# Performance work log

Measured on AMD Instinct MI355X. Metric: run time of the kernel, lower is better.

The kernel has to match this reference:

```python
import jax, jax.numpy as jnp
import numpy as np

N_NODES = 100000
N_EDGES = 3200000
IN_DIM, HID_DIM, OUT_DIM = 128, 64, 2


def setup_inputs() -> dict:
    key = jax.random.key(0)
    k1, k2, k3, k4 = jax.random.split(key, 4)
    x = jax.random.normal(k1, (N_NODES, IN_DIM), dtype=jnp.float32)
    edge_index = jax.random.randint(k2, (2, N_EDGES), 0, N_NODES, dtype=jnp.int64)
    # GCNConv weights (glorot-style scale) and zero biases
    W1 = jax.random.normal(k3, (IN_DIM, HID_DIM), dtype=jnp.float32) / np.sqrt(IN_DIM)
    b1 = jnp.zeros((HID_DIM,), dtype=jnp.float32)
    W2 = jax.random.normal(k4, (HID_DIM, OUT_DIM), dtype=jnp.float32) / np.sqrt(HID_DIM)
    b2 = jnp.zeros((OUT_DIM,), dtype=jnp.float32)
    return {"x": x, "edge_index": edge_index, "W1": W1, "b1": b1, "W2": W2, "b2": b2}


def _gcn_norm(edge_index, num_nodes):
    # PyG GCNConv default: add self-loops, symmetric normalization deg^-1/2.
    loops = jnp.arange(num_nodes, dtype=edge_index.dtype)
    src = jnp.concatenate([edge_index[0], loops])  # [E+N]
    dst = jnp.concatenate([edge_index[1], loops])  # [E+N]
    deg = jax.ops.segment_sum(jnp.ones_like(dst, dtype=jnp.float32), dst,
                              num_segments=num_nodes)  # in-degree incl. self-loop
    dinv = jnp.where(deg > 0, jax.lax.rsqrt(deg), 0.0)
    norm = dinv[src] * dinv[dst]  # [E+N]
    return src, dst, norm


def _gcn_conv(h, W, b, src, dst, norm, num_nodes):
    h = h @ W                              # dense transform first (smaller dim)
    msg = h[src] * norm[:, None]           # gather + scale: [E+N, d]
    out = jax.ops.segment_sum(msg, dst, num_segments=num_nodes)  # scatter-add
    return out + b


def reference(x, edge_index, W1, b1, W2, b2):
    n = x.shape[0]
    src, dst, norm = _gcn_norm(edge_index, n)
    h = _gcn_conv(x, W1, b1, src, dst, norm, n)
    h = jax.nn.relu(h)
    return _gcn_conv(h, W2, b2, src, dst, norm, n)
```

## Files before the change

kernel.cpp:

```cpp
#include <hip/hip_runtime.h>
#include <hip/hip_bf16.h>


#define N_NODES 100000
#define IN_DIM 128
#define HID_DIM 64
#define OUT_DIM 2
#define NB 391
#define BCAP 12288
#define CROUNDS 12
#define CHUNK 8192
#define ZROW N_NODES

typedef short bf16x8 __attribute__((ext_vector_type(8)));
typedef float f32x4 __attribute__((ext_vector_type(4)));

__device__ __forceinline__ unsigned short f2bf(float x) {
    unsigned int u = __float_as_uint(x);
    unsigned int r = (u + 0x7FFFu + ((u >> 16) & 1u)) >> 16;
    return (unsigned short)r;
}
__device__ __forceinline__ float bflo(unsigned int u) { return __uint_as_float(u << 16); }
__device__ __forceinline__ float bfhi(unsigned int u) { return __uint_as_float(u & 0xFFFF0000u); }
__device__ __forceinline__ f32x4 vlo(uint4 r) {
    return (f32x4){bflo(r.x), bflo(r.y), bflo(r.z), bflo(r.w)};
}
__device__ __forceinline__ f32x4 vhi(uint4 r) {
    return (f32x4){bfhi(r.x), bfhi(r.y), bfhi(r.z), bfhi(r.w)};
}
__device__ __forceinline__ int wave_incl_scan(int v, int laneid) {
#pragma unroll
    for (int off = 1; off < 64; off <<= 1) {
        int u = __shfl_up(v, off);
        if (laneid >= off) v += u;
    }
    return v;
}

__global__ __launch_bounds__(512) void part_kernel(const int* __restrict__ ei,
                                                   int* __restrict__ gCursor,
                                                   int* __restrict__ part, int E) {
    __shared__ int hist[512], lrow[512], gbase[512], lcur[512];
    __shared__ int lpk[CHUNK];
    __shared__ short lbkt[CHUNK];
    __shared__ int wsum[8], wofs[8];
    const int t = threadIdx.x;
    const int lane = t & 63, wv = t >> 6;
    const int base = blockIdx.x * CHUNK;
    const int cntC = min(CHUNK, E - base);

    hist[t] = 0;
    __syncthreads();

    int s[16], d[16];
    bool val[16];
    if (base + CHUNK <= E) {
#pragma unroll
        for (int i = 0; i < 4; ++i) {
            int4 sv = ((const int4*)(ei + base))[t + i * 512];
            int4 dv = ((const int4*)(ei + E + base))[t + i * 512];
            s[i * 4 + 0] = sv.x; s[i * 4 + 1] = sv.y; s[i * 4 + 2] = sv.z; s[i * 4 + 3] = sv.w;
            d[i * 4 + 0] = dv.x; d[i * 4 + 1] = dv.y; d[i * 4 + 2] = dv.z; d[i * 4 + 3] = dv.w;
            val[i * 4 + 0] = val[i * 4 + 1] = val[i * 4 + 2] = val[i * 4 + 3] = true;
        }
    } else {
#pragma unroll
        for (int i = 0; i < 16; ++i) {
            int e = base + t + i * 512;
            val[i] = (e < E);
            if (val[i]) {
                s[i] = ei[e];
                d[i] = ei[E + e];
            }
        }
    }
#pragma unroll
    for (int i = 0; i < 16; ++i)
        if (val[i]) atomicAdd(&hist[d[i] >> 8], 1);
    __syncthreads();

    int v = hist[t];
    int inc = wave_incl_scan(v, lane);
    if (lane == 63) wsum[wv] = inc;
    __syncthreads();
    if (t < 64) {
        int w = (t < 8) ? wsum[t] : 0;
        int wi = wave_incl_scan(w, t);
        if (t < 8) wofs[t] = wi - w;
    }
    __syncthreads();
    int excl = inc - v + wofs[wv];
    if (t < NB && v > 0) {
        int old = atomicAdd(&gCursor[t], v);
        gbase[t] = t * BCAP + old;
    }
    lcur[t] = excl;
    lrow[t] = excl;
    __syncthreads();

#pragma unroll
    for (int i = 0; i < 16; ++i) {
        if (val[i]) {
            int b = d[i] >> 8;
            int pos = atomicAdd(&lcur[b], 1);
            lpk[pos] = s[i] | ((d[i] & 255) << 20);
            lbkt[pos] = (short)b;
        }
    }
    __syncthreads();

    for (int i = t; i < cntC; i += 512) {
        int b = lbkt[i];
        int g = gbase[b] + (i - lrow[b]);
        if (g < (b + 1) * BCAP)
            part[g] = lpk[i];
    }
}

__global__ __launch_bounds__(1024) void csr_kernel(const int* __restrict__ part,
                                                   const int* __restrict__ gCursor,
                                                   int* __restrict__ cnt,
                                                   float* __restrict__ dinv,
                                                   int* __restrict__ rowptr,
                                                   int* __restrict__ csr_src, int n) {
    __shared__ int wcnt[16][256];
    __shared__ int wsum[4], wofs[4];
    const int b = blockIdx.x, t = threadIdx.x;
    const int lane = t & 63, wv = t >> 6;
    const int start = b * BCAP;
    const int count = min(gCursor[b], BCAP);

    for (int i = t; i < 16 * 256; i += 1024) ((int*)wcnt)[i] = 0;
    __syncthreads();

    int pk[CROUNDS];
    bool val[CROUNDS];
#pragma unroll
    for (int k = 0; k < CROUNDS; ++k) {
        int i = t + k * 1024;
        val[k] = (i < count);
        pk[k] = val[k] ? part[start + i] : 0;
        if (val[k]) atomicAdd(&wcnt[wv][(pk[k] >> 20) & 255], 1);
    }
    __syncthreads();

    int v = 0, pv = 0;
    if (t < 256) {
        int sum = 0;
#pragma unroll
        for (int w = 0; w < 16; ++w) sum += wcnt[w][t];
        v = sum;
        pv = (v + 7) & ~7;
    }
    int inc = 0;
    if (t < 256) {
        inc = wave_incl_scan(pv, lane);
        if (lane == 63) wsum[wv] = inc;
    }
    __syncthreads();
    if (t < 64) {
        int w = (t < 4) ? wsum[t] : 0;
        int wi = wave_incl_scan(w, t);
        if (t < 4) wofs[t] = wi - w;
    }
    __syncthreads();
    if (t < 256) {
        int excl = inc - pv + wofs[wv];
        int node = (b << 8) + t;
        if (node < n) {
            cnt[node] = v;
            dinv[node] = rsqrtf((float)v + 1.0f);
            rowptr[node] = start + excl;
        }
        for (int j = v; j < pv; ++j) csr_src[start + excl + j] = ZROW;
        int run = excl;
#pragma unroll
        for (int w = 0; w < 16; ++w) {
            int c = wcnt[w][t];
            wcnt[w][t] = run;
            run += c;
        }
    }
    __syncthreads();

#pragma unroll
    for (int k = 0; k < CROUNDS; ++k) {
        if (val[k]) {
            int pos = atomicAdd(&wcnt[wv][(pk[k] >> 20) & 255], 1);
            csr_src[start + pos] = pk[k] & 0xFFFFF;
        }
    }
}

__global__ __launch_bounds__(256) void gemm1_kernel(const float* __restrict__ x,
                                                    const float* __restrict__ W1,
                                                    const float* __restrict__ dinv,
                                                    unsigned short* __restrict__ hsb, int n) {
    __shared__ unsigned short sX[64 * 136];
    __shared__ unsigned short sW[64 * 136];
    const int tid = threadIdx.x;
    const int rbase = blockIdx.x * 64;

    if (blockIdx.x == 0 && tid < 8)
        ((float4*)&hsb[(unsigned)ZROW * HID_DIM])[tid] = make_float4(0.f, 0.f, 0.f, 0.f);

    for (int i = tid; i < 2048; i += 256) {
        int k = i >> 4, cq = (i & 15) << 2;
        float4 v = ((const float4*)W1)[i];
        sW[(cq + 0) * 136 + k] = f2bf(v.x);
        sW[(cq + 1) * 136 + k] = f2bf(v.y);
        sW[(cq + 2) * 136 + k] = f2bf(v.z);
        sW[(cq + 3) * 136 + k] = f2bf(v.w);
    }
    for (int i = tid; i < 2048; i += 256) {
        int r = i >> 5, kq = (i & 31) << 2;
        int gr = rbase + r;
        float4 v = make_float4(0.f, 0.f, 0.f, 0.f);
        if (gr < n) v = ((const float4*)x)[gr * 32 + (i & 31)];
        ushort4 u;
        u.x = f2bf(v.x); u.y = f2bf(v.y); u.z = f2bf(v.z); u.w = f2bf(v.w);
        *(ushort4*)&sX[r * 136 + kq] = u;
    }
    __syncthreads();

    const int wave = tid >> 6, lane = tid & 63;
    const int quad = lane >> 4, l16 = lane & 15;
    const int rowoff = wave * 16;

    f32x4 acc[4];
#pragma unroll
    for (int t = 0; t < 4; ++t) acc[t] = (f32x4){0.f, 0.f, 0.f, 0.f};

#pragma unroll
    for (int k0 = 0; k0 < 128; k0 += 32) {
        bf16x8 a = *(const bf16x8*)&sX[(rowoff + l16) * 136 + k0 + quad * 8];
#pragma unroll
        for (int t = 0; t < 4; ++t) {
            bf16x8 b = *(const bf16x8*)&sW[(t * 16 + l16) * 136 + k0 + quad * 8];
            acc[t] = __builtin_amdgcn_mfma_f32_16x16x32_bf16(a, b, acc[t], 0, 0, 0);
        }
    }

#pragma unroll
    for (int r = 0; r < 4; ++r) {
        int grow = rbase + rowoff + quad * 4 + r;
        if (grow < n) {
            float di = dinv[grow];
#pragma unroll
            for (int t = 0; t < 4; ++t)
                hsb[grow * HID_DIM + t * 16 + l16] = f2bf(acc[t][r] * di);
        }
    }
}

__global__ __launch_bounds__(256) void agg1_kernel(const int* __restrict__ rowptr,
                                                   const int* __restrict__ cnt,
                                                   const int* __restrict__ csr_src,
                                                   const unsigned short* __restrict__ hsb,
                                                   const float* __restrict__ dinv,
                                                   const float* __restrict__ b1,
                                                   const float* __restrict__ W2,
                                                   float* __restrict__ hs2, int n) {
    const int node = blockIdx.x * 32 + (threadIdx.x >> 3);
    const int l = threadIdx.x & 7;
    const unsigned lofs = (unsigned)l * 8;
    const int start = rowptr[node];
    const int deg = cnt[node];
    const int iters = (deg + 7) >> 3;

    f32x4 alo = (f32x4){0.f, 0.f, 0.f, 0.f};
    f32x4 ahi = (f32x4){0.f, 0.f, 0.f, 0.f};

    const int4* qp = (const int4*)(csr_src + start);
    int4 ia = make_int4(ZROW, ZROW, ZROW, ZROW), ib = ia;
    if (iters > 0) { ia = qp[0]; ib = qp[1]; }
    for (int it = 0; it < iters; ++it) {
        const bool more = (it + 1 < iters);
        int4 na = more ? qp[2 * it + 2] : make_int4(ZROW, ZROW, ZROW, ZROW);
        int4 nb = more ? qp[2 * it + 3] : make_int4(ZROW, ZROW, ZROW, ZROW);
        uint4 r0 = *(const uint4*)&hsb[(unsigned)ia.x * HID_DIM + lofs];
        uint4 r1 = *(const uint4*)&hsb[(unsigned)ia.y * HID_DIM + lofs];
        uint4 r2 = *(const uint4*)&hsb[(unsigned)ia.z * HID_DIM + lofs];
        uint4 r3 = *(const uint4*)&hsb[(unsigned)ia.w * HID_DIM + lofs];
        uint4 r4 = *(const uint4*)&hsb[(unsigned)ib.x * HID_DIM + lofs];
        uint4 r5 = *(const uint4*)&hsb[(unsigned)ib.y * HID_DIM + lofs];
        uint4 r6 = *(const uint4*)&hsb[(unsigned)ib.z * HID_DIM + lofs];
        uint4 r7 = *(const uint4*)&hsb[(unsigned)ib.w * HID_DIM + lofs];
        alo += vlo(r0);  ahi += vhi(r0);
        alo += vlo(r1);  ahi += vhi(r1);
        alo += vlo(r2);  ahi += vhi(r2);
        alo += vlo(r3);  ahi += vhi(r3);
        alo += vlo(r4);  ahi += vhi(r4);
        alo += vlo(r5);  ahi += vhi(r5);
        alo += vlo(r6);  ahi += vhi(r6);
        alo += vlo(r7);  ahi += vhi(r7);
        ia = na; ib = nb;
    }

    float a[8];
    a[0] = alo[0]; a[1] = ahi[0]; a[2] = alo[1]; a[3] = ahi[1];
    a[4] = alo[2]; a[5] = ahi[2]; a[6] = alo[3]; a[7] = ahi[3];

    {
        uint4 raw = *(const uint4*)&hsb[(unsigned)node * HID_DIM + lofs];
        a[0] += bflo(raw.x); a[1] += bfhi(raw.x);
        a[2] += bflo(raw.y); a[3] += bfhi(raw.y);
        a[4] += bflo(raw.z); a[5] += bfhi(raw.z);
        a[6] += bflo(raw.w); a[7] += bfhi(raw.w);
    }

    float di = dinv[node];
    float4 bb0 = *(const float4*)&b1[l * 8];
    float4 bb1 = *(const float4*)&b1[l * 8 + 4];
    float t0 = fmaxf(fmaf(di, a[0], bb0.x), 0.0f);
    float t1 = fmaxf(fmaf(di, a[1], bb0.y), 0.0f);
    float t2 = fmaxf(fmaf(di, a[2], bb0.z), 0.0f);
    float t3 = fmaxf(fmaf(di, a[3], bb0.w), 0.0f);
    float t4 = fmaxf(fmaf(di, a[4], bb1.x), 0.0f);
    float t5 = fmaxf(fmaf(di, a[5], bb1.y), 0.0f);
    float t6 = fmaxf(fmaf(di, a[6], bb1.z), 0.0f);
    float t7 = fmaxf(fmaf(di, a[7], bb1.w), 0.0f);

    float4 w0 = *(const float4*)&W2[l * 16];
    float4 w1 = *(const float4*)&W2[l * 16 + 4];
    float4 w2 = *(const float4*)&W2[l * 16 + 8];
    float4 w3 = *(const float4*)&W2[l * 16 + 12];
    float p0 = t0 * w0.x + t1 * w0.z + t2 * w1.x + t3 * w1.z
             + t4 * w2.x + t5 * w2.z + t6 * w3.x + t7 * w3.z;
    float p1 = t0 * w0.y + t1 * w0.w + t2 * w1.y + t3 * w1.w
             + t4 * w2.y + t5 * w2.w + t6 * w3.y + t7 * w3.w;
    p0 += __shfl_xor(p0, 1);  p1 += __shfl_xor(p1, 1);
    p0 += __shfl_xor(p0, 2);  p1 += __shfl_xor(p1, 2);
    p0 += __shfl_xor(p0, 4);  p1 += __shfl_xor(p1, 4);

    if (l == 0) {
        *(float2*)&hs2[node * OUT_DIM] = make_float2(di * p0, di * p1);
    }
}

__global__ __launch_bounds__(256) void agg2_kernel(const int* __restrict__ rowptr,
                                                   const int* __restrict__ cnt,
                                                   const int* __restrict__ csr_src,
                                                   const float* __restrict__ hs2,
                                                   const float* __restrict__ dinv,
                                                   const float* __restrict__ b2,
                                                   float* __restrict__ out, int n) {
    int node = blockIdx.x * 16 + (threadIdx.x >> 4);
    int lane = threadIdx.x & 15;
    int start = rowptr[node];
    int deg = cnt[node];

    float a0 = 0.0f, a1 = 0.0f;
    for (int j = lane; j < deg; j += 16) {
        int s = csr_src[start + j];
        float2 v = *(const float2*)&hs2[s * OUT_DIM];
        a0 += v.x;
        a1 += v.y;
    }
#pragma unroll
    for (int off = 8; off > 0; off >>= 1) {
        a0 += __shfl_xor(a0, off);
        a1 += __shfl_xor(a1, off);
    }
    if (lane == 0) {
        float di = dinv[node];
        float2 self = *(const float2*)&hs2[node * OUT_DIM];
        out[node * OUT_DIM + 0] = di * (a0 + self.x) + b2[0];
        out[node * OUT_DIM + 1] = di * (a1 + self.y) + b2[1];
    }
}

extern "C" void kernel_launch(void* const* d_in, const int* in_sizes, int n_in,
                              void* d_out, int out_size, void* d_ws, size_t ws_size,
                              hipStream_t stream) {
    const float* x  = (const float*)d_in[0];
    const int*   ei = (const int*)d_in[1];
    const float* W1 = (const float*)d_in[2];
    const float* b1 = (const float*)d_in[3];
    const float* W2 = (const float*)d_in[4];
    const float* b2 = (const float*)d_in[5];
    float* out = (float*)d_out;

    const int n = N_NODES;
    const int E = in_sizes[1] / 2;

    char* ws = (char*)d_ws;
    int*   gCursor = (int*)  (ws + 0);
    int*   cnt     = (int*)  (ws + (1u << 20));
    float* dinv    = (float*)(ws + (2u << 20));
    int*   rowptr  = (int*)  (ws + (3u << 20));
    float* hs2     = (float*)(ws + (4u << 20));
    int*   part    = (int*)  (ws + (5u << 20));
    unsigned short* hsb = (unsigned short*)(ws + (5u << 20));
    int*   csr_src = (int*)  (ws + (25u << 20));

    hipMemsetAsync(gCursor, 0, NB * sizeof(int), stream);

    part_kernel<<<(E + CHUNK - 1) / CHUNK, 512, 0, stream>>>(ei, gCursor, part, E);
    csr_kernel<<<NB, 1024, 0, stream>>>(part, gCursor, cnt, dinv, rowptr, csr_src, n);

    gemm1_kernel<<<(n + 63) / 64, 256, 0, stream>>>(x, W1, dinv, hsb, n);
    agg1_kernel<<<n / 32, 256, 0, stream>>>(rowptr, cnt, csr_src, hsb, dinv, b1, W2, hs2, n);
    agg2_kernel<<<n / 16, 256, 0, stream>>>(rowptr, cnt, csr_src, hs2, dinv, b2, out, n);
}
```

Baseline: 232.2 us.

## Sort nodes by degree within block and widen agg1 gather to 16 edges

Inside agg1, each block now bitonic-sorts its 32 nodes by degree so that nodes with similar degree share a wavefront, which cuts divergence from uneven trip counts. The gather loop also handles 16 neighbour rows per iteration instead of 8, with CSR row padding raised to multiples of 16 to match. This puts more loads in flight per iteration. The cost is extra padding entries that point at the zero row, more register pressure, and a small sort plus block barrier per block.

```diff
diff --git a/kernel.cpp b/kernel.cpp
--- a/kernel.cpp
+++ b/kernel.cpp
@@ -150,7 +150,7 @@
 #pragma unroll
         for (int w = 0; w < 16; ++w) sum += wcnt[w][t];
         v = sum;
-        pv = (v + 7) & ~7;
+        pv = (v + 15) & ~15;
     }
     int inc = 0;
     if (t < 256) {
@@ -261,23 +261,49 @@
                                                    const float* __restrict__ b1,
                                                    const float* __restrict__ W2,
                                                    float* __restrict__ hs2, int n) {
-    const int node = blockIdx.x * 32 + (threadIdx.x >> 3);
-    const int l = threadIdx.x & 7;
+    __shared__ int sid[32];
+    const int tid = threadIdx.x;
+    const int nbase = blockIdx.x * 32;
+
+    if (tid < 32) {
+        int nd = nbase + tid;
+        int key = min(cnt[nd], 1023);
+        int v = (key << 17) | nd;
+#pragma unroll
+        for (int k = 2; k <= 32; k <<= 1) {
+#pragma unroll
+            for (int j = k >> 1; j > 0; j >>= 1) {
+                int u = __shfl_xor(v, j);
+                bool asc = ((tid & k) == 0);
+                bool low = ((tid & j) == 0);
+                int mn = min(v, u), mx = max(v, u);
+                v = (asc == low) ? mn : mx;
+            }
+        }
+        sid[tid] = v & 0x1FFFF;
+    }
+    __syncthreads();
+
+    const int node = sid[tid >> 3];
+    const int l = tid & 7;
     const unsigned lofs = (unsigned)l * 8;
     const int start = rowptr[node];
     const int deg = cnt[node];
-    const int iters = (deg + 7) >> 3;
+    const int iters = (deg + 15) >> 4;
 
     f32x4 alo = (f32x4){0.f, 0.f, 0.f, 0.f};
     f32x4 ahi = (f32x4){0.f, 0.f, 0.f, 0.f};
 
+    const int4 Z4 = make_int4(ZROW, ZROW, ZROW, ZROW);
     const int4* qp = (const int4*)(csr_src + start);
-    int4 ia = make_int4(ZROW, ZROW, ZROW, ZROW), ib = ia;
-    if (iters > 0) { ia = qp[0]; ib = qp[1]; }
+    int4 ia = Z4, ib = Z4, ic = Z4, id = Z4;
+    if (iters > 0) { ia = qp[0]; ib = qp[1]; ic = qp[2]; id = qp[3]; }
     for (int it = 0; it < iters; ++it) {
         const bool more = (it + 1 < iters);
-        int4 na = more ? qp[2 * it + 2] : make_int4(ZROW, ZROW, ZROW, ZROW);
-        int4 nb = more ? qp[2 * it + 3] : make_int4(ZROW, ZROW, ZROW, ZROW);
+        int4 na = more ? qp[4 * it + 4] : Z4;
+        int4 nb = more ? qp[4 * it + 5] : Z4;
+        int4 nc = more ? qp[4 * it + 6] : Z4;
+        int4 nd = more ? qp[4 * it + 7] : Z4;
         uint4 r0 = *(const uint4*)&hsb[(unsigned)ia.x * HID_DIM + lofs];
         uint4 r1 = *(const uint4*)&hsb[(unsigned)ia.y * HID_DIM + lofs];
         uint4 r2 = *(const uint4*)&hsb[(unsigned)ia.z * HID_DIM + lofs];
@@ -286,6 +312,14 @@
         uint4 r5 = *(const uint4*)&hsb[(unsigned)ib.y * HID_DIM + lofs];
         uint4 r6 = *(const uint4*)&hsb[(unsigned)ib.z * HID_DIM + lofs];
         uint4 r7 = *(const uint4*)&hsb[(unsigned)ib.w * HID_DIM + lofs];
+        uint4 r8 = *(const uint4*)&hsb[(unsigned)ic.x * HID_DIM + lofs];
+        uint4 r9 = *(const uint4*)&hsb[(unsigned)ic.y * HID_DIM + lofs];
+        uint4 rA = *(const uint4*)&hsb[(unsigned)ic.z * HID_DIM + lofs];
+        uint4 rB = *(const uint4*)&hsb[(unsigned)ic.w * HID_DIM + lofs];
+        uint4 rC = *(const uint4*)&hsb[(unsigned)id.x * HID_DIM + lofs];
+        uint4 rD = *(const uint4*)&hsb[(unsigned)id.y * HID_DIM + lofs];
+        uint4 rE = *(const uint4*)&hsb[(unsigned)id.z * HID_DIM + lofs];
+        uint4 rF = *(const uint4*)&hsb[(unsigned)id.w * HID_DIM + lofs];
         alo += vlo(r0);  ahi += vhi(r0);
         alo += vlo(r1);  ahi += vhi(r1);
         alo += vlo(r2);  ahi += vhi(r2);
@@ -294,7 +328,15 @@
         alo += vlo(r5);  ahi += vhi(r5);
         alo += vlo(r6);  ahi += vhi(r6);
         alo += vlo(r7);  ahi += vhi(r7);
-        ia = na; ib = nb;
+        alo += vlo(r8);  ahi += vhi(r8);
+        alo += vlo(r9);  ahi += vhi(r9);
+        alo += vlo(rA);  ahi += vhi(rA);
+        alo += vlo(rB);  ahi += vhi(rB);
+        alo += vlo(rC);  ahi += vhi(rC);
+        alo += vlo(rD);  ahi += vhi(rD);
+        alo += vlo(rE);  ahi += vhi(rE);
+        alo += vlo(rF);  ahi += vhi(rF);
+        ia = na; ib = nb; ic = nc; id = nd;
     }
 
     float a[8];
```

Result: no change. 234.9 us (+1.2%).

## Replace two-pass bucket partition CSR build with global-atomic degree count and scatter

Applied to the files above, without the earlier changes.

Replaces the shared-memory bucketed partition and per-bucket CSR kernels with a global-atomic in-degree count, a per-bucket scan for row pointers, and a global-atomic cursor scatter of source indices. The dinv array is dropped and recomputed from cnt in each consumer with rsqrt. This removes the intermediate partition buffer and its extra read/write pass. In exchange it puts 6.4M contended global atomics and random scattered writes on the critical path. It also makes the neighbour order within each row nondeterministic, which can change floating-point summation order.

```diff
diff --git a/kernel.cpp b/kernel.cpp
--- a/kernel.cpp
+++ b/kernel.cpp
@@ -6,10 +6,8 @@
 #define IN_DIM 128
 #define HID_DIM 64
 #define OUT_DIM 2
-#define NB 391
+#define NBKT 391
 #define BCAP 12288
-#define CROUNDS 12
-#define CHUNK 8192
 #define ZROW N_NODES
 
 typedef short bf16x8 __attribute__((ext_vector_type(8)));
@@ -22,12 +20,6 @@
 }
 __device__ __forceinline__ float bflo(unsigned int u) { return __uint_as_float(u << 16); }
 __device__ __forceinline__ float bfhi(unsigned int u) { return __uint_as_float(u & 0xFFFF0000u); }
-__device__ __forceinline__ f32x4 vlo(uint4 r) {
-    return (f32x4){bflo(r.x), bflo(r.y), bflo(r.z), bflo(r.w)};
-}
-__device__ __forceinline__ f32x4 vhi(uint4 r) {
-    return (f32x4){bfhi(r.x), bfhi(r.y), bfhi(r.z), bfhi(r.w)};
-}
 __device__ __forceinline__ int wave_incl_scan(int v, int laneid) {
 #pragma unroll
     for (int off = 1; off < 64; off <<= 1) {
@@ -37,126 +29,35 @@
     return v;
 }
 
-__global__ __launch_bounds__(512) void part_kernel(const int* __restrict__ ei,
-                                                   int* __restrict__ gCursor,
-                                                   int* __restrict__ part, int E) {
-    __shared__ int hist[512], lrow[512], gbase[512], lcur[512];
-    __shared__ int lpk[CHUNK];
-    __shared__ short lbkt[CHUNK];
-    __shared__ int wsum[8], wofs[8];
-    const int t = threadIdx.x;
-    const int lane = t & 63, wv = t >> 6;
-    const int base = blockIdx.x * CHUNK;
-    const int cntC = min(CHUNK, E - base);
-
-    hist[t] = 0;
-    __syncthreads();
-
-    int s[16], d[16];
-    bool val[16];
-    if (base + CHUNK <= E) {
-#pragma unroll
-        for (int i = 0; i < 4; ++i) {
-            int4 sv = ((const int4*)(ei + base))[t + i * 512];
-            int4 dv = ((const int4*)(ei + E + base))[t + i * 512];
-            s[i * 4 + 0] = sv.x; s[i * 4 + 1] = sv.y; s[i * 4 + 2] = sv.z; s[i * 4 + 3] = sv.w;
-            d[i * 4 + 0] = dv.x; d[i * 4 + 1] = dv.y; d[i * 4 + 2] = dv.z; d[i * 4 + 3] = dv.w;
-            val[i * 4 + 0] = val[i * 4 + 1] = val[i * 4 + 2] = val[i * 4 + 3] = true;
-        }
-    } else {
-#pragma unroll
-        for (int i = 0; i < 16; ++i) {
-            int e = base + t + i * 512;
-            val[i] = (e < E);
-            if (val[i]) {
-                s[i] = ei[e];
-                d[i] = ei[E + e];
-            }
-        }
-    }
-#pragma unroll
-    for (int i = 0; i < 16; ++i)
-        if (val[i]) atomicAdd(&hist[d[i] >> 8], 1);
-    __syncthreads();
-
-    int v = hist[t];
-    int inc = wave_incl_scan(v, lane);
-    if (lane == 63) wsum[wv] = inc;
-    __syncthreads();
-    if (t < 64) {
-        int w = (t < 8) ? wsum[t] : 0;
-        int wi = wave_incl_scan(w, t);
-        if (t < 8) wofs[t] = wi - w;
-    }
-    __syncthreads();
-    int excl = inc - v + wofs[wv];
-    if (t < NB && v > 0) {
-        int old = atomicAdd(&gCursor[t], v);
-        gbase[t] = t * BCAP + old;
-    }
-    lcur[t] = excl;
-    lrow[t] = excl;
-    __syncthreads();
-
-#pragma unroll
-    for (int i = 0; i < 16; ++i) {
-        if (val[i]) {
-            int b = d[i] >> 8;
-            int pos = atomicAdd(&lcur[b], 1);
-            lpk[pos] = s[i] | ((d[i] & 255) << 20);
-            lbkt[pos] = (short)b;
-        }
-    }
-    __syncthreads();
-
-    for (int i = t; i < cntC; i += 512) {
-        int b = lbkt[i];
-        int g = gbase[b] + (i - lrow[b]);
-        if (g < (b + 1) * BCAP)
-            part[g] = lpk[i];
-    }
-}
-
-__global__ __launch_bounds__(1024) void csr_kernel(const int* __restrict__ part,
-                                                   const int* __restrict__ gCursor,
-                                                   int* __restrict__ cnt,
-                                                   float* __restrict__ dinv,
+__global__ __launch_bounds__(256) void deg_kernel(const int* __restrict__ ei,
+                                                  int* __restrict__ cnt, int E) {
+    const int idx = blockIdx.x * 256 + threadIdx.x;
+    const int stride = gridDim.x * 256;
+    const int4* dp = (const int4*)(ei + E);
+    const int nq = E >> 2;
+    for (int i = idx; i < nq; i += stride) {
+        int4 d = dp[i];
+        atomicAdd(&cnt[d.x], 1);
+        atomicAdd(&cnt[d.y], 1);
+        atomicAdd(&cnt[d.z], 1);
+        atomicAdd(&cnt[d.w], 1);
+    }
+    for (int e = (E & ~3) + idx; e < E; e += stride)
+        atomicAdd(&cnt[ei[E + e]], 1);
+}
+
+__global__ __launch_bounds__(256) void scan_kernel(const int* __restrict__ cnt,
                                                    int* __restrict__ rowptr,
+                                                   int* __restrict__ cursor,
                                                    int* __restrict__ csr_src, int n) {
-    __shared__ int wcnt[16][256];
     __shared__ int wsum[4], wofs[4];
     const int b = blockIdx.x, t = threadIdx.x;
+    const int node = (b << 8) + t;
     const int lane = t & 63, wv = t >> 6;
-    const int start = b * BCAP;
-    const int count = min(gCursor[b], BCAP);
-
-    for (int i = t; i < 16 * 256; i += 1024) ((int*)wcnt)[i] = 0;
-    __syncthreads();
-
-    int pk[CROUNDS];
-    bool val[CROUNDS];
-#pragma unroll
-    for (int k = 0; k < CROUNDS; ++k) {
-        int i = t + k * 1024;
-        val[k] = (i < count);
-        pk[k] = val[k] ? part[start + i] : 0;
-        if (val[k]) atomicAdd(&wcnt[wv][(pk[k] >> 20) & 255], 1);
-    }
-    __syncthreads();
-
-    int v = 0, pv = 0;
-    if (t < 256) {
-        int sum = 0;
-#pragma unroll
-        for (int w = 0; w < 16; ++w) sum += wcnt[w][t];
-        v = sum;
-        pv = (v + 7) & ~7;
-    }
-    int inc = 0;
-    if (t < 256) {
-        inc = wave_incl_scan(pv, lane);
-        if (lane == 63) wsum[wv] = inc;
-    }
+    const int v = (node < n) ? cnt[node] : 0;
+    const int pv = (v + 7) & ~7;
+    int inc = wave_incl_scan(pv, lane);
+    if (lane == 63) wsum[wv] = inc;
     __syncthreads();
     if (t < 64) {
         int w = (t < 4) ? wsum[t] : 0;
@@ -164,37 +65,45 @@
         if (t < 4) wofs[t] = wi - w;
     }
     __syncthreads();
-    if (t < 256) {
-        int excl = inc - pv + wofs[wv];
-        int node = (b << 8) + t;
-        if (node < n) {
-            cnt[node] = v;
-            dinv[node] = rsqrtf((float)v + 1.0f);
-            rowptr[node] = start + excl;
-        }
-        for (int j = v; j < pv; ++j) csr_src[start + excl + j] = ZROW;
-        int run = excl;
-#pragma unroll
-        for (int w = 0; w < 16; ++w) {
-            int c = wcnt[w][t];
-            wcnt[w][t] = run;
-            run += c;
-        }
-    }
-    __syncthreads();
-
-#pragma unroll
-    for (int k = 0; k < CROUNDS; ++k) {
-        if (val[k]) {
-            int pos = atomicAdd(&wcnt[wv][(pk[k] >> 20) & 255], 1);
-            csr_src[start + pos] = pk[k] & 0xFFFFF;
-        }
+    if (node < n) {
+        const int excl = inc - pv + wofs[wv];
+        const int base = b * BCAP + excl;
+        rowptr[node] = base;
+        cursor[node] = base;
+        for (int j = v; j < pv; ++j) csr_src[base + j] = ZROW;
+    }
+}
+
+__global__ __launch_bounds__(256) void scatter_kernel(const int* __restrict__ ei,
+                                                      int* __restrict__ cursor,
+                                                      int* __restrict__ csr_src, int E) {
+    const int idx = blockIdx.x * 256 + threadIdx.x;
+    const int stride = gridDim.x * 256;
+    const int4* sp = (const int4*)ei;
+    const int4* dp = (const int4*)(ei + E);
+    const int nq = E >> 2;
+    for (int i = idx; i < nq; i += stride) {
+        int4 s = sp[i];
+        int4 d = dp[i];
+        int p0 = atomicAdd(&cursor[d.x], 1);
+        int p1 = atomicAdd(&cursor[d.y], 1);
+        int p2 = atomicAdd(&cursor[d.z], 1);
+        int p3 = atomicAdd(&cursor[d.w], 1);
+        if (p0 < ((d.x >> 8) + 1) * BCAP) csr_src[p0] = s.x;
+        if (p1 < ((d.y >> 8) + 1) * BCAP) csr_src[p1] = s.y;
+        if (p2 < ((d.z >> 8) + 1) * BCAP) csr_src[p2] = s.z;
+        if (p3 < ((d.w >> 8) + 1) * BCAP) csr_src[p3] = s.w;
+    }
+    for (int e = (E & ~3) + idx; e < E; e += stride) {
+        int s = ei[e], d = ei[E + e];
+        int p = atomicAdd(&cursor[d], 1);
+        if (p < ((d >> 8) + 1) * BCAP) csr_src[p] = s;
     }
 }
 
 __global__ __launch_bounds__(256) void gemm1_kernel(const float* __restrict__ x,
                                                     const float* __restrict__ W1,
-                                                    const float* __restrict__ dinv,
+                                                    const int* __restrict__ cnt,
                                                     unsigned short* __restrict__ hsb, int n) {
     __shared__ unsigned short sX[64 * 136];
     __shared__ unsigned short sW[64 * 136];
@@ -245,7 +154,7 @@
     for (int r = 0; r < 4; ++r) {
         int grow = rbase + rowoff + quad * 4 + r;
         if (grow < n) {
-            float di = dinv[grow];
+            float di = rsqrtf((float)cnt[grow] + 1.0f);
 #pragma unroll
             for (int t = 0; t < 4; ++t)
                 hsb[grow * HID_DIM + t * 16 + l16] = f2bf(acc[t][r] * di);
@@ -257,7 +166,6 @@
                                                    const int* __restrict__ cnt,
                                                    const int* __restrict__ csr_src,
                                                    const unsigned short* __restrict__ hsb,
-                                                   const float* __restrict__ dinv,
                                                    const float* __restrict__ b1,
                                                    const float* __restrict__ W2,
                                                    float* __restrict__ hs2, int n) {
@@ -286,14 +194,22 @@
         uint4 r5 = *(const uint4*)&hsb[(unsigned)ib.y * HID_DIM + lofs];
         uint4 r6 = *(const uint4*)&hsb[(unsigned)ib.z * HID_DIM + lofs];
         uint4 r7 = *(const uint4*)&hsb[(unsigned)ib.w * HID_DIM + lofs];
-        alo += vlo(r0);  ahi += vhi(r0);
-        alo += vlo(r1);  ahi += vhi(r1);
-        alo += vlo(r2);  ahi += vhi(r2);
-        alo += vlo(r3);  ahi += vhi(r3);
-        alo += vlo(r4);  ahi += vhi(r4);
-        alo += vlo(r5);  ahi += vhi(r5);
-        alo += vlo(r6);  ahi += vhi(r6);
-        alo += vlo(r7);  ahi += vhi(r7);
+        alo += (f32x4){bflo(r0.x), bflo(r0.y), bflo(r0.z), bflo(r0.w)};
+        ahi += (f32x4){bfhi(r0.x), bfhi(r0.y), bfhi(r0.z), bfhi(r0.w)};
+        alo += (f32x4){bflo(r1.x), bflo(r1.y), bflo(r1.z), bflo(r1.w)};
+        ahi += (f32x4){bfhi(r1.x), bfhi(r1.y), bfhi(r1.z), bfhi(r1.w)};
+        alo += (f32x4){bflo(r2.x), bflo(r2.y), bflo(r2.z), bflo(r2.w)};
+        ahi += (f32x4){bfhi(r2.x), bfhi(r2.y), bfhi(r2.z), bfhi(r2.w)};
+        alo += (f32x4){bflo(r3.x), bflo(r3.y), bflo(r3.z), bflo(r3.w)};
+        ahi += (f32x4){bfhi(r3.x), bfhi(r3.y), bfhi(r3.z), bfhi(r3.w)};
+        alo += (f32x4){bflo(r4.x), bflo(r4.y), bflo(r4.z), bflo(r4.w)};
+        ahi += (f32x4){bfhi(r4.x), bfhi(r4.y), bfhi(r4.z), bfhi(r4.w)};
+        alo += (f32x4){bflo(r5.x), bflo(r5.y), bflo(r5.z), bflo(r5.w)};
+        ahi += (f32x4){bfhi(r5.x), bfhi(r5.y), bfhi(r5.z), bfhi(r5.w)};
+        alo += (f32x4){bflo(r6.x), bflo(r6.y), bflo(r6.z), bflo(r6.w)};
+        ahi += (f32x4){bfhi(r6.x), bfhi(r6.y), bfhi(r6.z), bfhi(r6.w)};
+        alo += (f32x4){bflo(r7.x), bflo(r7.y), bflo(r7.z), bflo(r7.w)};
+        ahi += (f32x4){bfhi(r7.x), bfhi(r7.y), bfhi(r7.z), bfhi(r7.w)};
         ia = na; ib = nb;
     }
 
@@ -309,7 +225,7 @@
         a[6] += bflo(raw.w); a[7] += bfhi(raw.w);
     }
 
-    float di = dinv[node];
+    const float di = rsqrtf((float)deg + 1.0f);
     float4 bb0 = *(const float4*)&b1[l * 8];
     float4 bb1 = *(const float4*)&b1[l * 8 + 4];
     float t0 = fmaxf(fmaf(di, a[0], bb0.x), 0.0f);
@@ -342,7 +258,6 @@
                                                    const int* __restrict__ cnt,
                                                    const int* __restrict__ csr_src,
                                                    const float* __restrict__ hs2,
-                                                   const float* __restrict__ dinv,
                                                    const float* __restrict__ b2,
                                                    float* __restrict__ out, int n) {
     int node = blockIdx.x * 16 + (threadIdx.x >> 4);
@@ -363,7 +278,7 @@
         a1 += __shfl_xor(a1, off);
     }
     if (lane == 0) {
-        float di = dinv[node];
+        float di = rsqrtf((float)deg + 1.0f);
         float2 self = *(const float2*)&hs2[node * OUT_DIM];
         out[node * OUT_DIM + 0] = di * (a0 + self.x) + b2[0];
         out[node * OUT_DIM + 1] = di * (a1 + self.y) + b2[1];
@@ -385,21 +300,19 @@
     const int E = in_sizes[1] / 2;
 
     char* ws = (char*)d_ws;
-    int*   gCursor = (int*)  (ws + 0);
-    int*   cnt     = (int*)  (ws + (1u << 20));
-    float* dinv    = (float*)(ws + (2u << 20));
-    int*   rowptr  = (int*)  (ws + (3u << 20));
-    float* hs2     = (float*)(ws + (4u << 20));
-    int*   part    = (int*)  (ws + (5u << 20));
-    unsigned short* hsb = (unsigned short*)(ws + (5u << 20));
-    int*   csr_src = (int*)  (ws + (25u << 20));
-
-    hipMemsetAsync(gCursor, 0, NB * sizeof(int), stream);
-
-    part_kernel<<<(E + CHUNK - 1) / CHUNK, 512, 0, stream>>>(ei, gCursor, part, E);
-    csr_kernel<<<NB, 1024, 0, stream>>>(part, gCursor, cnt, dinv, rowptr, csr_src, n);
-
-    gemm1_kernel<<<(n + 63) / 64, 256, 0, stream>>>(x, W1, dinv, hsb, n);
-    agg1_kernel<<<n / 32, 256, 0, stream>>>(rowptr, cnt, csr_src, hsb, dinv, b1, W2, hs2, n);
-    agg2_kernel<<<n / 16, 256, 0, stream>>>(rowptr, cnt, csr_src, hs2, dinv, b2, out, n);
-}
+    int*   cnt     = (int*)  (ws + 0);
+    int*   rowptr  = (int*)  (ws + (1u << 20));
+    int*   cursor  = (int*)  (ws + (2u << 20));
+    float* hs2     = (float*)(ws + (3u << 20));
+    int*   csr_src = (int*)  (ws + (4u << 20));
+    unsigned short* hsb = (unsigned short*)(ws + (24u << 20));
+
+    hipMemsetAsync(cnt, 0, N_NODES * sizeof(int), stream);
+
+    deg_kernel<<<2048, 256, 0, stream>>>(ei, cnt, E);
+    scan_kernel<<<NBKT, 256, 0, stream>>>(cnt, rowptr, cursor, csr_src, n);
+    gemm1_kernel<<<(n + 63) / 64, 256, 0, stream>>>(x, W1, cnt, hsb, n);
+    scatter_kernel<<<2048, 256, 0, stream>>>(ei, cursor, csr_src, E);
+    agg1_kernel<<<n / 32, 256, 0, stream>>>(rowptr, cnt, csr_src, hsb, b1, W2, hs2, n);
+    agg2_kernel<<<n / 16, 256, 0, stream>>>(rowptr, cnt, csr_src, hs2, b2, out, n);
+}
```

Measured after the change: 593.2 us. 155% more time.

## Degree-sort nodes per bucket for agg1 balance, reuse atomic ranks, recompute dinv

Applied to the files above, without the earlier changes.

Inside each 256-node bucket, csr_kernel now bitonic-sorts nodes by degree and writes a sortid permutation. agg1 uses it so the 8-lane groups in a wave handle nodes of similar degree, which is meant to cut divergence and load imbalance. The ranks returned by the first atomicAdd in part_kernel and csr_kernel are kept, so the second atomic scatter pass is no longer needed. The dinv array is dropped and rsqrt(deg+1) is recomputed from cnt wherever it is used. In exchange, csr_kernel gains an extra shared-memory sort with many barriers, and csr_src writes within a bucket now depend on atomic order.

```diff
diff --git a/kernel.cpp b/kernel.cpp
--- a/kernel.cpp
+++ b/kernel.cpp
@@ -6,7 +6,7 @@
 #define IN_DIM 128
 #define HID_DIM 64
 #define OUT_DIM 2
-#define NB 391
+#define NBKT 391
 #define BCAP 12288
 #define CROUNDS 12
 #define CHUNK 8192
@@ -22,12 +22,6 @@
 }
 __device__ __forceinline__ float bflo(unsigned int u) { return __uint_as_float(u << 16); }
 __device__ __forceinline__ float bfhi(unsigned int u) { return __uint_as_float(u & 0xFFFF0000u); }
-__device__ __forceinline__ f32x4 vlo(uint4 r) {
-    return (f32x4){bflo(r.x), bflo(r.y), bflo(r.z), bflo(r.w)};
-}
-__device__ __forceinline__ f32x4 vhi(uint4 r) {
-    return (f32x4){bfhi(r.x), bfhi(r.y), bfhi(r.z), bfhi(r.w)};
-}
 __device__ __forceinline__ int wave_incl_scan(int v, int laneid) {
 #pragma unroll
     for (int off = 1; off < 64; off <<= 1) {
@@ -40,7 +34,7 @@
 __global__ __launch_bounds__(512) void part_kernel(const int* __restrict__ ei,
                                                    int* __restrict__ gCursor,
                                                    int* __restrict__ part, int E) {
-    __shared__ int hist[512], lrow[512], gbase[512], lcur[512];
+    __shared__ int hist[512], lrow[512], gbase[512];
     __shared__ int lpk[CHUNK];
     __shared__ short lbkt[CHUNK];
     __shared__ int wsum[8], wofs[8];
@@ -52,7 +46,7 @@
     hist[t] = 0;
     __syncthreads();
 
-    int s[16], d[16];
+    int s[16], d[16], rk[16];
     bool val[16];
     if (base + CHUNK <= E) {
 #pragma unroll
@@ -76,7 +70,7 @@
     }
 #pragma unroll
     for (int i = 0; i < 16; ++i)
-        if (val[i]) atomicAdd(&hist[d[i] >> 8], 1);
+        if (val[i]) rk[i] = atomicAdd(&hist[d[i] >> 8], 1);
     __syncthreads();
 
     int v = hist[t];
@@ -89,12 +83,11 @@
         if (t < 8) wofs[t] = wi - w;
     }
     __syncthreads();
-    int excl = inc - v + wofs[wv];
-    if (t < NB && v > 0) {
+    const int excl = inc - v + wofs[wv];
+    if (t < NBKT && v > 0) {
         int old = atomicAdd(&gCursor[t], v);
         gbase[t] = t * BCAP + old;
     }
-    lcur[t] = excl;
     lrow[t] = excl;
     __syncthreads();
 
@@ -102,7 +95,7 @@
     for (int i = 0; i < 16; ++i) {
         if (val[i]) {
             int b = d[i] >> 8;
-            int pos = atomicAdd(&lcur[b], 1);
+            int pos = lrow[b] + rk[i];
             lpk[pos] = s[i] | ((d[i] & 255) << 20);
             lbkt[pos] = (short)b;
         }
@@ -120,11 +113,12 @@
 __global__ __launch_bounds__(1024) void csr_kernel(const int* __restrict__ part,
                                                    const int* __restrict__ gCursor,
                                                    int* __restrict__ cnt,
-                                                   float* __restrict__ dinv,
                                                    int* __restrict__ rowptr,
+                                                   int* __restrict__ sortid,
                                                    int* __restrict__ csr_src, int n) {
     __shared__ int wcnt[16][256];
     __shared__ int wsum[4], wofs[4];
+    __shared__ int sv[256];
     const int b = blockIdx.x, t = threadIdx.x;
     const int lane = t & 63, wv = t >> 6;
     const int start = b * BCAP;
@@ -133,14 +127,14 @@
     for (int i = t; i < 16 * 256; i += 1024) ((int*)wcnt)[i] = 0;
     __syncthreads();
 
-    int pk[CROUNDS];
+    int pk[CROUNDS], rk[CROUNDS];
     bool val[CROUNDS];
 #pragma unroll
     for (int k = 0; k < CROUNDS; ++k) {
         int i = t + k * 1024;
         val[k] = (i < count);
         pk[k] = val[k] ? part[start + i] : 0;
-        if (val[k]) atomicAdd(&wcnt[wv][(pk[k] >> 20) & 255], 1);
+        if (val[k]) rk[k] = atomicAdd(&wcnt[wv][(pk[k] >> 20) & 255], 1);
     }
     __syncthreads();
 
@@ -165,11 +159,10 @@
     }
     __syncthreads();
     if (t < 256) {
-        int excl = inc - pv + wofs[wv];
-        int node = (b << 8) + t;
+        const int excl = inc - pv + wofs[wv];
+        const int node = (b << 8) + t;
         if (node < n) {
             cnt[node] = v;
-            dinv[node] = rsqrtf((float)v + 1.0f);
             rowptr[node] = start + excl;
         }
         for (int j = v; j < pv; ++j) csr_src[start + excl + j] = ZROW;
@@ -180,21 +173,41 @@
             wcnt[w][t] = run;
             run += c;
         }
-    }
+        int key = (node < n) ? min(v, 4095) : 0;
+        sv[t] = (key << 8) | t;
+    }
+    __syncthreads();
+
+#pragma unroll
+    for (int k = 2; k <= 256; k <<= 1) {
+#pragma unroll
+        for (int j = k >> 1; j > 0; j >>= 1) {
+            if (t < 256) {
+                int ixj = t ^ j;
+                if (ixj > t) {
+                    int a = sv[t], c2 = sv[ixj];
+                    bool asc = ((t & k) == 0);
+                    if (asc ? (a > c2) : (a < c2)) { sv[t] = c2; sv[ixj] = a; }
+                }
+            }
+            __syncthreads();
+        }
+    }
+    if (t < 256) sortid[(b << 8) + t] = (b << 8) + (sv[t] & 255);
     __syncthreads();
 
 #pragma unroll
     for (int k = 0; k < CROUNDS; ++k) {
         if (val[k]) {
-            int pos = atomicAdd(&wcnt[wv][(pk[k] >> 20) & 255], 1);
-            csr_src[start + pos] = pk[k] & 0xFFFFF;
+            int nodelo = (pk[k] >> 20) & 255;
+            csr_src[start + wcnt[wv][nodelo] + rk[k]] = pk[k] & 0xFFFFF;
         }
     }
 }
 
 __global__ __launch_bounds__(256) void gemm1_kernel(const float* __restrict__ x,
                                                     const float* __restrict__ W1,
-                                                    const float* __restrict__ dinv,
+                                                    const int* __restrict__ cnt,
                                                     unsigned short* __restrict__ hsb, int n) {
     __shared__ unsigned short sX[64 * 136];
     __shared__ unsigned short sW[64 * 136];
@@ -245,7 +258,7 @@
     for (int r = 0; r < 4; ++r) {
         int grow = rbase + rowoff + quad * 4 + r;
         if (grow < n) {
-            float di = dinv[grow];
+            float di = rsqrtf((float)cnt[grow] + 1.0f);
 #pragma unroll
             for (int t = 0; t < 4; ++t)
                 hsb[grow * HID_DIM + t * 16 + l16] = f2bf(acc[t][r] * di);
@@ -255,13 +268,15 @@
 
 __global__ __launch_bounds__(256) void agg1_kernel(const int* __restrict__ rowptr,
                                                    const int* __restrict__ cnt,
+                                                   const int* __restrict__ sortid,
                                                    const int* __restrict__ csr_src,
                                                    const unsigned short* __restrict__ hsb,
-                                                   const float* __restrict__ dinv,
                                                    const float* __restrict__ b1,
                                                    const float* __restrict__ W2,
                                                    float* __restrict__ hs2, int n) {
-    const int node = blockIdx.x * 32 + (threadIdx.x >> 3);
+    const int slot = blockIdx.x * 32 + (threadIdx.x >> 3);
+    const int node = sortid[slot];
+    if (node >= n) return;
     const int l = threadIdx.x & 7;
     const unsigned lofs = (unsigned)l * 8;
     const int start = rowptr[node];
@@ -286,14 +301,22 @@
         uint4 r5 = *(const uint4*)&hsb[(unsigned)ib.y * HID_DIM + lofs];
         uint4 r6 = *(const uint4*)&hsb[(unsigned)ib.z * HID_DIM + lofs];
         uint4 r7 = *(const uint4*)&hsb[(unsigned)ib.w * HID_DIM + lofs];
-        alo += vlo(r0);  ahi += vhi(r0);
-        alo += vlo(r1);  ahi += vhi(r1);
-        alo += vlo(r2);  ahi += vhi(r2);
-        alo += vlo(r3);  ahi += vhi(r3);
-        alo += vlo(r4);  ahi += vhi(r4);
-        alo += vlo(r5);  ahi += vhi(r5);
-        alo += vlo(r6);  ahi += vhi(r6);
-        alo += vlo(r7);  ahi += vhi(r7);
+        alo += (f32x4){bflo(r0.x), bflo(r0.y), bflo(r0.z), bflo(r0.w)};
+        ahi += (f32x4){bfhi(r0.x), bfhi(r0.y), bfhi(r0.z), bfhi(r0.w)};
+        alo += (f32x4){bflo(r1.x), bflo(r1.y), bflo(r1.z), bflo(r1.w)};
+        ahi += (f32x4){bfhi(r1.x), bfhi(r1.y), bfhi(r1.z), bfhi(r1.w)};
+        alo += (f32x4){bflo(r2.x), bflo(r2.y), bflo(r2.z), bflo(r2.w)};
+        ahi += (f32x4){bfhi(r2.x), bfhi(r2.y), bfhi(r2.z), bfhi(r2.w)};
+        alo += (f32x4){bflo(r3.x), bflo(r3.y), bflo(r3.z), bflo(r3.w)};
+        ahi += (f32x4){bfhi(r3.x), bfhi(r3.y), bfhi(r3.z), bfhi(r3.w)};
+        alo += (f32x4){bflo(r4.x), bflo(r4.y), bflo(r4.z), bflo(r4.w)};
+        ahi += (f32x4){bfhi(r4.x), bfhi(r4.y), bfhi(r4.z), bfhi(r4.w)};
+        alo += (f32x4){bflo(r5.x), bflo(r5.y), bflo(r5.z), bflo(r5.w)};
+        ahi += (f32x4){bfhi(r5.x), bfhi(r5.y), bfhi(r5.z), bfhi(r5.w)};
+        alo += (f32x4){bflo(r6.x), bflo(r6.y), bflo(r6.z), bflo(r6.w)};
+        ahi += (f32x4){bfhi(r6.x), bfhi(r6.y), bfhi(r6.z), bfhi(r6.w)};
+        alo += (f32x4){bflo(r7.x), bflo(r7.y), bflo(r7.z), bflo(r7.w)};
+        ahi += (f32x4){bfhi(r7.x), bfhi(r7.y), bfhi(r7.z), bfhi(r7.w)};
         ia = na; ib = nb;
     }
 
@@ -309,7 +332,7 @@
         a[6] += bflo(raw.w); a[7] += bfhi(raw.w);
     }
 
-    float di = dinv[node];
+    const float di = rsqrtf((float)deg + 1.0f);
     float4 bb0 = *(const float4*)&b1[l * 8];
     float4 bb1 = *(const float4*)&b1[l * 8 + 4];
     float t0 = fmaxf(fmaf(di, a[0], bb0.x), 0.0f);
@@ -342,7 +365,6 @@
                                                    const int* __restrict__ cnt,
                                                    const int* __restrict__ csr_src,
                                                    const float* __restrict__ hs2,
-                                                   const float* __restrict__ dinv,
                                                    const float* __restrict__ b2,
                                                    float* __restrict__ out, int n) {
     int node = blockIdx.x * 16 + (threadIdx.x >> 4);
@@ -363,7 +385,7 @@
         a1 += __shfl_xor(a1, off);
     }
     if (lane == 0) {
-        float di = dinv[node];
+        float di = rsqrtf((float)deg + 1.0f);
         float2 self = *(const float2*)&hs2[node * OUT_DIM];
         out[node * OUT_DIM + 0] = di * (a0 + self.x) + b2[0];
         out[node * OUT_DIM + 1] = di * (a1 + self.y) + b2[1];
@@ -387,19 +409,19 @@
     char* ws = (char*)d_ws;
     int*   gCursor = (int*)  (ws + 0);
     int*   cnt     = (int*)  (ws + (1u << 20));
-    float* dinv    = (float*)(ws + (2u << 20));
-    int*   rowptr  = (int*)  (ws + (3u << 20));
+    int*   rowptr  = (int*)  (ws + (2u << 20));
+    int*   sortid  = (int*)  (ws + (3u << 20));
     float* hs2     = (float*)(ws + (4u << 20));
     int*   part    = (int*)  (ws + (5u << 20));
     unsigned short* hsb = (unsigned short*)(ws + (5u << 20));
     int*   csr_src = (int*)  (ws + (25u << 20));
 
-    hipMemsetAsync(gCursor, 0, NB * sizeof(int), stream);
+    hipMemsetAsync(gCursor, 0, NBKT * sizeof(int), stream);
 
     part_kernel<<<(E + CHUNK - 1) / CHUNK, 512, 0, stream>>>(ei, gCursor, part, E);
-    csr_kernel<<<NB, 1024, 0, stream>>>(part, gCursor, cnt, dinv, rowptr, csr_src, n);
-
-    gemm1_kernel<<<(n + 63) / 64, 256, 0, stream>>>(x, W1, dinv, hsb, n);
-    agg1_kernel<<<n / 32, 256, 0, stream>>>(rowptr, cnt, csr_src, hsb, dinv, b1, W2, hs2, n);
-    agg2_kernel<<<n / 16, 256, 0, stream>>>(rowptr, cnt, csr_src, hs2, dinv, b2, out, n);
-}
+    csr_kernel<<<NBKT, 1024, 0, stream>>>(part, gCursor, cnt, rowptr, sortid, csr_src, n);
+
+    gemm1_kernel<<<(n + 63) / 64, 256, 0, stream>>>(x, W1, cnt, hsb, n);
+    agg1_kernel<<<NBKT * 8, 256, 0, stream>>>(rowptr, cnt, sortid, csr_src, hsb, b1, W2, hs2, n);
+    agg2_kernel<<<(n + 15) / 16, 256, 0, stream>>>(rowptr, cnt, csr_src, hs2, b2, out, n);
+}
```

Result: slower. 244.9 us (+5.5%).
